# Optimization experiments

Hardware: AMD Instinct MI355X
Metric: run time of the kernel (lower is better)

The kernel has to match this reference:

```python
import jax, jax.numpy as jnp
import numpy as np

# MX microscaling spec: block_size=32 shared power-of-2 scale, int8 elements (MXINT8),
# vector (SIMD) ops rounded to bfloat16 as in microxcaling's simd_* / vec_* ops.
BLOCK = 32
BITS = 8  # int8 element format: grid step 2^(shared_exp - (BITS-2)), range [-2^(BITS-1), 2^(BITS-1)-1]


def bf16_round(x):
    # bfloat=16 rounding used by simd_split / simd_add / vec ops
    return x.astype(jnp.bfloat16).astype(jnp.float32)


def mx_quant(x):
    """MXINT8 fake-quant along last (contraction) axis with block-shared exponent.
    Straight-through estimator for gradients."""
    s = x.shape
    xb = x.reshape(s[:-1] + (s[-1] // BLOCK, BLOCK))
    amax = jnp.max(jnp.abs(xb), axis=-1, keepdims=True)
    shared_exp = jnp.floor(jnp.log2(jnp.where(amax > 0, amax, 1.0)))
    scale = jnp.exp2(shared_exp - (BITS - 2))
    q = jnp.clip(jnp.round(xb / scale), -(2.0 ** (BITS - 1)), 2.0 ** (BITS - 1) - 1) * scale
    q = jnp.where(amax > 0, q, 0.0).reshape(s)
    return x + jax.lax.stop_gradient(q - x)


def mx_linear(x, W, b):
    # quantize activations and weights to MX blocks along K, fp32 accumulate, bf16 bias-add
    y = jnp.einsum('btk,ok->bto', mx_quant(x), mx_quant(W))
    return bf16_round(y + b)


def mx_layernorm(x, w, b, eps=1e-5):
    mu = jnp.mean(x, axis=-1, keepdims=True)
    var = jnp.mean(jnp.square(x - mu), axis=-1, keepdims=True)
    return bf16_round((x - mu) * jax.lax.rsqrt(var + eps) * w + b)


def mx_gelu(x):
    # tanh-approx gelu as in microxcaling, bf16-rounded output
    c = jnp.float32(0.7978845608028654)  # sqrt(2/pi)
    return bf16_round(0.5 * x * (1.0 + jnp.tanh(c * (x + 0.044715 * x * x * x))))


def setup_inputs() -> dict:
    key = jax.random.key(0)
    ks = jax.random.split(key, 5)
    B, S, H = 2, 2048, 2048
    inputs = jax.random.normal(ks[0], (B, S, H), dtype=jnp.float32)
    ln_w = jnp.ones((H,), dtype=jnp.float32)
    ln_b = jnp.zeros((H,), dtype=jnp.float32)
    W1 = jax.random.normal(ks[1], (4 * H, H), dtype=jnp.float32) * (1.0 / np.sqrt(H))
    b1 = jnp.zeros((4 * H,), dtype=jnp.float32)
    W2 = jax.random.normal(ks[2], (H, 4 * H), dtype=jnp.float32) * (1.0 / np.sqrt(4 * H))
    b2 = jnp.zeros((H,), dtype=jnp.float32)
    return {"inputs": inputs, "ln_w": ln_w, "ln_b": ln_b, "W1": W1, "b1": b1, "W2": W2, "b2": b2}


def reference(inputs, ln_w, ln_b, W1, b1, W2, b2):
    # simd_split: bf16-rounded copies for MLP branch and residual branch
    x = bf16_round(inputs)
    residual = bf16_round(inputs)
    h = mx_layernorm(x, ln_w, ln_b)
    h = mx_linear(h, W1, b1)          # [B,S,4H]
    h = mx_gelu(h)
    h = mx_linear(h, W2, b2)          # [B,S,H]
    return bf16_round(residual + h)    # simd_add
```

## Files before the change

### kernel.cpp

```cpp
#include <hip/hip_runtime.h>

#define DEVI __device__ __forceinline__

typedef __bf16 bf16x8 __attribute__((ext_vector_type(8)));
typedef float f32x4 __attribute__((ext_vector_type(4)));

DEVI unsigned short f2bf(float f) {
  unsigned u = __float_as_uint(f);
  u = (u + 0x7FFFu + ((u >> 16) & 1u)) >> 16;
  return (unsigned short)u;
}
DEVI float bf2f(unsigned short h) { return __uint_as_float(((unsigned)h) << 16); }
DEVI float bf16r(float f) { return bf2f(f2bf(f)); }

DEVI void quant8(const float* h, float amax, unsigned short* q) {
  if (amax > 0.f) {
    int e;
    (void)frexpf(amax, &e);
    float scale = ldexpf(1.0f, e - 7);
    float inv   = ldexpf(1.0f, 7 - e);
#pragma unroll
    for (int k = 0; k < 8; ++k) {
      float qv = rintf(h[k] * inv);
      qv = fminf(fmaxf(qv, -128.f), 127.f);
      q[k] = f2bf(qv * scale);
    }
  } else {
#pragma unroll
    for (int k = 0; k < 8; ++k) q[k] = 0;
  }
}

DEVI void gl2lds16(const void* g, void* l) {
  __builtin_amdgcn_global_load_lds(
      (__attribute__((address_space(1))) void*)const_cast<void*>(g),
      (__attribute__((address_space(3))) void*)l, 16, 0, 0);
}

__global__ __launch_bounds__(256) void quant_f32_k(const float* __restrict__ X,
                                                   unsigned short* __restrict__ Q) {
  size_t idx = (size_t)blockIdx.x * 256 + threadIdx.x;
  float4 v0 = ((const float4*)X)[idx * 2];
  float4 v1 = ((const float4*)X)[idx * 2 + 1];
  float h[8] = {v0.x, v0.y, v0.z, v0.w, v1.x, v1.y, v1.z, v1.w};
  float amax = 0.f;
#pragma unroll
  for (int k = 0; k < 8; ++k) amax = fmaxf(amax, fabsf(h[k]));
  amax = fmaxf(amax, __shfl_xor(amax, 1));
  amax = fmaxf(amax, __shfl_xor(amax, 2));
  unsigned short q[8];
  quant8(h, amax, q);
  uint4 o;
  o.x = (unsigned)q[0] | ((unsigned)q[1] << 16);
  o.y = (unsigned)q[2] | ((unsigned)q[3] << 16);
  o.z = (unsigned)q[4] | ((unsigned)q[5] << 16);
  o.w = (unsigned)q[6] | ((unsigned)q[7] << 16);
  ((uint4*)Q)[idx] = o;
}

__global__ __launch_bounds__(256) void quant_bf16_ip(unsigned short* __restrict__ X) {
  size_t idx = (size_t)blockIdx.x * 256 + threadIdx.x;
  uint4 v = ((const uint4*)X)[idx];
  unsigned short u[8] = {(unsigned short)(v.x & 0xffff), (unsigned short)(v.x >> 16),
                         (unsigned short)(v.y & 0xffff), (unsigned short)(v.y >> 16),
                         (unsigned short)(v.z & 0xffff), (unsigned short)(v.z >> 16),
                         (unsigned short)(v.w & 0xffff), (unsigned short)(v.w >> 16)};
  float h[8];
#pragma unroll
  for (int k = 0; k < 8; ++k) h[k] = bf2f(u[k]);
  float amax = 0.f;
#pragma unroll
  for (int k = 0; k < 8; ++k) amax = fmaxf(amax, fabsf(h[k]));
  amax = fmaxf(amax, __shfl_xor(amax, 1));
  amax = fmaxf(amax, __shfl_xor(amax, 2));
  unsigned short q[8];
  quant8(h, amax, q);
  uint4 o;
  o.x = (unsigned)q[0] | ((unsigned)q[1] << 16);
  o.y = (unsigned)q[2] | ((unsigned)q[3] << 16);
  o.z = (unsigned)q[4] | ((unsigned)q[5] << 16);
  o.w = (unsigned)q[6] | ((unsigned)q[7] << 16);
  ((uint4*)X)[idx] = o;
}

__global__ __launch_bounds__(256) void ln_quant_k(const float* __restrict__ X,
                                                  const float* __restrict__ w,
                                                  const float* __restrict__ b,
                                                  unsigned short* __restrict__ out) {
  const int H = 2048;
  const int row = blockIdx.x;
  const int t = threadIdx.x;
  const int lane = t & 63, wave = t >> 6;
  const float* xr = X + (size_t)row * H;
  float4 v0 = ((const float4*)xr)[2 * t];
  float4 v1 = ((const float4*)xr)[2 * t + 1];
  float x[8] = {bf16r(v0.x), bf16r(v0.y), bf16r(v0.z), bf16r(v0.w),
                bf16r(v1.x), bf16r(v1.y), bf16r(v1.z), bf16r(v1.w)};
  __shared__ float red[4];
  float s = 0.f;
#pragma unroll
  for (int k = 0; k < 8; ++k) s += x[k];
#pragma unroll
  for (int o = 32; o; o >>= 1) s += __shfl_xor(s, o);
  if (lane == 0) red[wave] = s;
  __syncthreads();
  float mu = (red[0] + red[1] + red[2] + red[3]) * (1.0f / H);
  __syncthreads();
  float v = 0.f;
#pragma unroll
  for (int k = 0; k < 8; ++k) { float d = x[k] - mu; v += d * d; }
#pragma unroll
  for (int o = 32; o; o >>= 1) v += __shfl_xor(v, o);
  if (lane == 0) red[wave] = v;
  __syncthreads();
  float var = (red[0] + red[1] + red[2] + red[3]) * (1.0f / H);
  float rstd = 1.0f / sqrtf(var + 1e-5f);
  float h[8];
  float amax = 0.f;
#pragma unroll
  for (int k = 0; k < 8; ++k) {
    int col = t * 8 + k;
    h[k] = bf16r((x[k] - mu) * rstd * w[col] + b[col]);
    amax = fmaxf(amax, fabsf(h[k]));
  }
  amax = fmaxf(amax, __shfl_xor(amax, 1));
  amax = fmaxf(amax, __shfl_xor(amax, 2));
  unsigned short q[8];
  quant8(h, amax, q);
  uint4 o4;
  o4.x = (unsigned)q[0] | ((unsigned)q[1] << 16);
  o4.y = (unsigned)q[2] | ((unsigned)q[3] << 16);
  o4.z = (unsigned)q[4] | ((unsigned)q[5] << 16);
  o4.w = (unsigned)q[6] | ((unsigned)q[7] << 16);
  ((uint4*)(out + (size_t)row * H))[t] = o4;
}

template <int MODE>
__global__ __launch_bounds__(256) void gemm_mx(const unsigned short* __restrict__ A,
                                               const unsigned short* __restrict__ B,
                                               int M, int N, int K,
                                               const float* __restrict__ bias,
                                               const float* __restrict__ resid,
                                               void* __restrict__ outp) {
  __shared__ unsigned short As[128 * 64];
  __shared__ unsigned short Bs[128 * 64];

  const int tid = threadIdx.x;
  const int lane = tid & 63;
  const int wave = tid >> 6;
  const int wr = (wave >> 1) * 64;
  const int wc = (wave & 1) * 64;
  const int lr = lane & 15;
  const int quad = lane >> 4;

  const int m0 = blockIdx.y * 128;
  const int n0 = blockIdx.x * 128;

  size_t aoff[4], boff[4];
  int lbase[4];
#pragma unroll
  for (int j = 0; j < 4; ++j) {
    int n = j * 256 + tid;
    int r = n >> 3, c = (n & 7) ^ (r & 7);
    aoff[j] = (size_t)(m0 + r) * K + (size_t)c * 8;
    boff[j] = (size_t)(n0 + r) * K + (size_t)c * 8;
    lbase[j] = (j * 256 + (tid & ~63)) * 8;
  }

  f32x4 acc[4][4];
#pragma unroll
  for (int i = 0; i < 4; ++i)
#pragma unroll
    for (int j = 0; j < 4; ++j) acc[i][j] = (f32x4){0.f, 0.f, 0.f, 0.f};

  for (int k0 = 0; k0 < K; k0 += 64) {
#pragma unroll
    for (int j = 0; j < 4; ++j) gl2lds16(A + aoff[j] + k0, As + lbase[j]);
#pragma unroll
    for (int j = 0; j < 4; ++j) gl2lds16(B + boff[j] + k0, Bs + lbase[j]);
    __syncthreads();
#pragma unroll
    for (int s = 0; s < 2; ++s) {
      bf16x8 af[4], bfr[4];
#pragma unroll
      for (int i = 0; i < 4; ++i) {
        int row = wr + i * 16 + lr;
        int ch = (s * 4 + quad) ^ (row & 7);
        af[i] = *(const bf16x8*)(As + row * 64 + ch * 8);
      }
#pragma unroll
      for (int j = 0; j < 4; ++j) {
        int row = wc + j * 16 + lr;
        int ch = (s * 4 + quad) ^ (row & 7);
        bfr[j] = *(const bf16x8*)(Bs + row * 64 + ch * 8);
      }
#pragma unroll
      for (int i = 0; i < 4; ++i)
#pragma unroll
        for (int j = 0; j < 4; ++j)
          acc[i][j] = __builtin_amdgcn_mfma_f32_16x16x32_bf16(af[i], bfr[j], acc[i][j], 0, 0, 0);
    }
    __syncthreads();
  }

#pragma unroll
  for (int i = 0; i < 4; ++i) {
#pragma unroll
    for (int j = 0; j < 4; ++j) {
#pragma unroll
      for (int r = 0; r < 4; ++r) {
        int gm = m0 + wr + i * 16 + quad * 4 + r;
        int gn = n0 + wc + j * 16 + lr;
        float y = acc[i][j][r];
        if (MODE == 1) {
          float t = bf16r(y + bias[gn]);
          float u = 0.7978845608028654f * (t + 0.044715f * t * t * t);
          float g = 0.5f * t * (1.0f + tanhf(u));
          ((unsigned short*)outp)[(size_t)gm * N + gn] = f2bf(g);
        } else {
          float h = bf16r(y + bias[gn]);
          float rr = bf16r(resid[(size_t)gm * N + gn]);
          ((float*)outp)[(size_t)gm * N + gn] = bf16r(rr + h);
        }
      }
    }
  }
  (void)M;
}

extern "C" void kernel_launch(void* const* d_in, const int* in_sizes, int n_in,
                              void* d_out, int out_size, void* d_ws, size_t ws_size,
                              hipStream_t stream) {
  const float* inputs = (const float*)d_in[0];
  const float* ln_w   = (const float*)d_in[1];
  const float* ln_b   = (const float*)d_in[2];
  const float* W1     = (const float*)d_in[3];
  const float* b1     = (const float*)d_in[4];
  const float* W2     = (const float*)d_in[5];
  const float* b2     = (const float*)d_in[6];
  float* out = (float*)d_out;
  char* ws = (char*)d_ws;
  (void)in_sizes; (void)n_in; (void)out_size; (void)ws_size;

  unsigned short* qW1  = (unsigned short*)(ws);
  unsigned short* qW2  = (unsigned short*)(ws + (size_t)33554432);
  unsigned short* a1   = (unsigned short*)(ws + (size_t)67108864);
  unsigned short* act2 = (unsigned short*)(ws + (size_t)83886080);

  const int M = 4096;

  quant_f32_k<<<8192, 256, 0, stream>>>(W1, qW1);
  quant_f32_k<<<8192, 256, 0, stream>>>(W2, qW2);

  ln_quant_k<<<M, 256, 0, stream>>>(inputs, ln_w, ln_b, a1);

  gemm_mx<1><<<dim3(8192 / 128, M / 128), 256, 0, stream>>>(
      a1, qW1, M, 8192, 2048, b1, nullptr, (void*)act2);

  quant_bf16_ip<<<16384, 256, 0, stream>>>(act2);

  gemm_mx<2><<<dim3(2048 / 128, M / 128), 256, 0, stream>>>(
      act2, qW2, M, 2048, 8192, b2, inputs, (void*)out);
}
```

Before: 512.1 us.

## Fuse MX quantization of GELU activations into first GEMM epilogue

Removes the separate in-place quantization kernel over the 4096x8192 bf16 intermediate. The GEMM1 epilogue now does the MX block-amax reduction with cross-lane shuffles over 16-lane groups. Each 32-element block is covered by two j-columns across 16 lanes, and the epilogue quantizes before storing. It also replaces tanhf with an exp-based tanh and computes the scales with exponent bit arithmetic instead of frexpf/ldexpf. This saves a full read-write pass over the intermediate, at the cost of extra shuffles and registers in the epilogue. The exp-based tanh may differ slightly in precision from tanhf.

```diff
diff --git a/kernel.cpp b/kernel.cpp
--- a/kernel.cpp
+++ b/kernel.cpp
@@ -13,18 +13,24 @@
 DEVI float bf2f(unsigned short h) { return __uint_as_float(((unsigned)h) << 16); }
 DEVI float bf16r(float f) { return bf2f(f2bf(f)); }
 
+DEVI void mx_scales(float amax, float& scale, float& inv) {
+  unsigned eb = __float_as_uint(amax) & 0x7f800000u;
+  scale = __uint_as_float(eb - (6u << 23));
+  inv   = __uint_as_float((260u << 23) - eb);
+}
+
+DEVI unsigned short quantv(float v, float scale, float inv) {
+  float qv = rintf(v * inv);
+  qv = fminf(fmaxf(qv, -128.f), 127.f);
+  return f2bf(qv * scale);
+}
+
 DEVI void quant8(const float* h, float amax, unsigned short* q) {
   if (amax > 0.f) {
-    int e;
-    (void)frexpf(amax, &e);
-    float scale = ldexpf(1.0f, e - 7);
-    float inv   = ldexpf(1.0f, 7 - e);
-#pragma unroll
-    for (int k = 0; k < 8; ++k) {
-      float qv = rintf(h[k] * inv);
-      qv = fminf(fmaxf(qv, -128.f), 127.f);
-      q[k] = f2bf(qv * scale);
-    }
+    float scale, inv;
+    mx_scales(amax, scale, inv);
+#pragma unroll
+    for (int k = 0; k < 8; ++k) q[k] = quantv(h[k], scale, inv);
   } else {
 #pragma unroll
     for (int k = 0; k < 8; ++k) q[k] = 0;
@@ -56,31 +62,6 @@
   o.z = (unsigned)q[4] | ((unsigned)q[5] << 16);
   o.w = (unsigned)q[6] | ((unsigned)q[7] << 16);
   ((uint4*)Q)[idx] = o;
-}
-
-__global__ __launch_bounds__(256) void quant_bf16_ip(unsigned short* __restrict__ X) {
-  size_t idx = (size_t)blockIdx.x * 256 + threadIdx.x;
-  uint4 v = ((const uint4*)X)[idx];
-  unsigned short u[8] = {(unsigned short)(v.x & 0xffff), (unsigned short)(v.x >> 16),
-                         (unsigned short)(v.y & 0xffff), (unsigned short)(v.y >> 16),
-                         (unsigned short)(v.z & 0xffff), (unsigned short)(v.z >> 16),
-                         (unsigned short)(v.w & 0xffff), (unsigned short)(v.w >> 16)};
-  float h[8];
-#pragma unroll
-  for (int k = 0; k < 8; ++k) h[k] = bf2f(u[k]);
-  float amax = 0.f;
-#pragma unroll
-  for (int k = 0; k < 8; ++k) amax = fmaxf(amax, fabsf(h[k]));
-  amax = fmaxf(amax, __shfl_xor(amax, 1));
-  amax = fmaxf(amax, __shfl_xor(amax, 2));
-  unsigned short q[8];
-  quant8(h, amax, q);
-  uint4 o;
-  o.x = (unsigned)q[0] | ((unsigned)q[1] << 16);
-  o.y = (unsigned)q[2] | ((unsigned)q[3] << 16);
-  o.z = (unsigned)q[4] | ((unsigned)q[5] << 16);
-  o.w = (unsigned)q[6] | ((unsigned)q[7] << 16);
-  ((uint4*)X)[idx] = o;
 }
 
 __global__ __launch_bounds__(256) void ln_quant_k(const float* __restrict__ X,
@@ -203,22 +184,52 @@
     __syncthreads();
   }
 
-#pragma unroll
-  for (int i = 0; i < 4; ++i) {
-#pragma unroll
-    for (int j = 0; j < 4; ++j) {
+  if (MODE == 1) {
+#pragma unroll
+    for (int i = 0; i < 4; ++i) {
 #pragma unroll
       for (int r = 0; r < 4; ++r) {
-        int gm = m0 + wr + i * 16 + quad * 4 + r;
-        int gn = n0 + wc + j * 16 + lr;
-        float y = acc[i][j][r];
-        if (MODE == 1) {
-          float t = bf16r(y + bias[gn]);
-          float u = 0.7978845608028654f * (t + 0.044715f * t * t * t);
-          float g = 0.5f * t * (1.0f + tanhf(u));
-          ((unsigned short*)outp)[(size_t)gm * N + gn] = f2bf(g);
-        } else {
-          float h = bf16r(y + bias[gn]);
+        const int gm = m0 + wr + i * 16 + quad * 4 + r;
+        float g[4];
+#pragma unroll
+        for (int j = 0; j < 4; ++j) {
+          float t = bf16r(acc[i][j][r] + bias[n0 + wc + j * 16 + lr]);
+          float u2 = 1.5957691216057308f * (t + 0.044715f * t * t * t);
+          float E = __expf(u2);
+          float th = 1.0f - 2.0f / (E + 1.0f);
+          g[j] = bf16r(0.5f * t * (1.0f + th));
+        }
+        float a = fmaxf(fabsf(g[0]), fabsf(g[1]));
+        float b = fmaxf(fabsf(g[2]), fabsf(g[3]));
+#pragma unroll
+        for (int mset = 1; mset < 16; mset <<= 1) {
+          a = fmaxf(a, __shfl_xor(a, mset));
+          b = fmaxf(b, __shfl_xor(b, mset));
+        }
+        unsigned short q[4];
+        if (a > 0.f) {
+          float sc, iv; mx_scales(a, sc, iv);
+          q[0] = quantv(g[0], sc, iv); q[1] = quantv(g[1], sc, iv);
+        } else { q[0] = q[1] = 0; }
+        if (b > 0.f) {
+          float sc, iv; mx_scales(b, sc, iv);
+          q[2] = quantv(g[2], sc, iv); q[3] = quantv(g[3], sc, iv);
+        } else { q[2] = q[3] = 0; }
+        unsigned short* orow = (unsigned short*)outp + (size_t)gm * N + n0 + wc + lr;
+#pragma unroll
+        for (int j = 0; j < 4; ++j) orow[j * 16] = q[j];
+      }
+    }
+  } else {
+#pragma unroll
+    for (int i = 0; i < 4; ++i) {
+#pragma unroll
+      for (int j = 0; j < 4; ++j) {
+#pragma unroll
+        for (int r = 0; r < 4; ++r) {
+          int gm = m0 + wr + i * 16 + quad * 4 + r;
+          int gn = n0 + wc + j * 16 + lr;
+          float h = bf16r(acc[i][j][r] + bias[gn]);
           float rr = bf16r(resid[(size_t)gm * N + gn]);
           ((float*)outp)[(size_t)gm * N + gn] = bf16r(rr + h);
         }
@@ -257,8 +268,6 @@
   gemm_mx<1><<<dim3(8192 / 128, M / 128), 256, 0, stream>>>(
       a1, qW1, M, 8192, 2048, b1, nullptr, (void*)act2);
 
-  quant_bf16_ip<<<16384, 256, 0, stream>>>(act2);
-
   gemm_mx<2><<<dim3(2048 / 128, M / 128), 256, 0, stream>>>(
       act2, qW2, M, 2048, 8192, b2, inputs, (void*)out);
 }
```

After: 530.0 us. 1.03x slower.
